# Kernel optimization log

Hardware: AMD Instinct MI355X
Metric: run time of the kernel (lower is better)

## Reference

```python
import jax, jax.numpy as jnp
import numpy as np

B, N, C = 2, 2048, 1024
H, D = 16, 64  # num_heads, dim_head; H*D == C
SCALE = D ** -0.5


def setup_inputs() -> dict:
    key = jax.random.key(0)
    ks = jax.random.split(key, 5)
    x = jax.random.normal(ks[0], (B, N, C), dtype=jnp.float32)
    attn_bias = jax.random.normal(ks[1], (B, H, N, N), dtype=jnp.float32)
    Wq = jax.random.normal(ks[2], (C, C), dtype=jnp.float32) * (C ** -0.5)
    Wkv = jax.random.normal(ks[3], (2 * C, C), dtype=jnp.float32) * (C ** -0.5)
    Wo = jax.random.normal(ks[4], (C, C), dtype=jnp.float32) * (C ** -0.5)
    bo = jnp.zeros((C,), dtype=jnp.float32)
    return {"x": x, "attn_bias": attn_bias, "Wq": Wq, "Wkv": Wkv, "Wo": Wo, "bo": bo}


def reference(x, attn_bias, Wq, Wkv, Wo, bo):
    # QKV projections (torch Linear: y = x @ W.T)
    q = (x @ Wq.T).reshape(B, N, H, D)
    kv = x @ Wkv.T  # self-attention: context = x
    k, v = jnp.split(kv, 2, axis=-1)
    k = k.reshape(B, N, H, D)
    v = v.reshape(B, N, H, D)
    # scores: [B, H, N, N]
    sim = jnp.einsum('bnhd,bmhd->bhnm', q, k) * SCALE + attn_bias
    attn = jax.nn.softmax(sim, axis=-1)
    out = jnp.einsum('bhnm,bmhd->bnhd', attn, v).reshape(B, N, C)
    return out @ Wo.T + bo
```

## Files before the change

### kernel.cpp

```cpp
#include <hip/hip_runtime.h>
#include <stdint.h>

#define BB 2
#define NN 2048
#define CC 1024
#define HH 16
#define DD 64

typedef unsigned short ushort_t;
using u16x8  = __attribute__((ext_vector_type(8))) unsigned short;
using bf16x8 = __attribute__((ext_vector_type(8))) __bf16;
using f32x4  = __attribute__((ext_vector_type(4))) float;

__device__ __forceinline__ unsigned short f2b(float f) {
  union { float f; uint32_t u; } v; v.f = f;
  uint32_t u = v.u;
  return (unsigned short)((u + 0x7fffu + ((u >> 16) & 1u)) >> 16);
}

__device__ __forceinline__ f32x4 mfma_bf16(u16x8 a, u16x8 b, f32x4 c) {
  return __builtin_amdgcn_mfma_f32_16x16x32_bf16(
      __builtin_bit_cast(bf16x8, a), __builtin_bit_cast(bf16x8, b), c, 0, 0, 0);
}

#define GLD_LDS16(gp, lp)                                                        \
  __builtin_amdgcn_global_load_lds(                                              \
      (const __attribute__((address_space(1))) void*)(gp),                       \
      (__attribute__((address_space(3))) void*)(lp), 16, 0, 0)

__global__ void cast_all(const float* __restrict__ x, const float* __restrict__ wq,
                         const float* __restrict__ wkv, const float* __restrict__ wo,
                         ushort_t* __restrict__ xb, ushort_t* __restrict__ wqb,
                         ushort_t* __restrict__ wkvb, ushort_t* __restrict__ wob) {
  int c = blockIdx.x * 256 + threadIdx.x;
  const float* src; ushort_t* dst; int off;
  if (c < 1048576)      { src = x;   dst = xb;   off = c; }
  else if (c < 1310720) { src = wq;  dst = wqb;  off = c - 1048576; }
  else if (c < 1835008) { src = wkv; dst = wkvb; off = c - 1310720; }
  else                  { src = wo;  dst = wob;  off = c - 1835008; }
  float4 v = *(const float4*)(src + (size_t)off * 4);
  ushort4 o;
  o.x = f2b(v.x); o.y = f2b(v.y); o.z = f2b(v.z); o.w = f2b(v.w);
  *(ushort4*)(dst + (size_t)off * 4) = o;
}

template <bool F32OUT>
__launch_bounds__(256, 2)
__global__ void gemm_bt(const ushort_t* __restrict__ A, const ushort_t* __restrict__ Bw,
                        void* __restrict__ out, const float* __restrict__ bo,
                        int M, int Nf, int K) {
  __shared__ __align__(16) ushort_t As[128 * 64];
  __shared__ __align__(16) ushort_t Bs[128 * 64];
  const int tid = threadIdx.x;
  const int w = tid >> 6, l = tid & 63;
  const int quad = l >> 4, l15 = l & 15;
  const int m0 = blockIdx.y * 128, n0 = blockIdx.x * 128;
  const int wm = (w >> 1) * 64, wn = (w & 1) * 64;

  const f32x4 zero = {0.f, 0.f, 0.f, 0.f};
  f32x4 acc[4][4];
  for (int i = 0; i < 4; ++i)
    for (int j = 0; j < 4; ++j) acc[i][j] = zero;

  for (int k0 = 0; k0 < K; k0 += 64) {
#pragma unroll
    for (int i = 0; i < 4; ++i) {
      int q = (i * 4 + w) * 64 + l;
      int row = q >> 3, c8 = (q & 7) * 8;
      GLD_LDS16(A + (size_t)(m0 + row) * K + k0 + c8, As + (i * 4 + w) * 512);
      GLD_LDS16(Bw + (size_t)(n0 + row) * K + k0 + c8, Bs + (i * 4 + w) * 512);
    }
    __syncthreads();
#pragma unroll
    for (int s = 0; s < 2; ++s) {
      u16x8 af[4], bf[4];
#pragma unroll
      for (int mi = 0; mi < 4; ++mi)
        af[mi] = *(const u16x8*)(As + (wm + mi * 16 + l15) * 64 + s * 32 + quad * 8);
#pragma unroll
      for (int ni = 0; ni < 4; ++ni)
        bf[ni] = *(const u16x8*)(Bs + (wn + ni * 16 + l15) * 64 + s * 32 + quad * 8);
#pragma unroll
      for (int mi = 0; mi < 4; ++mi)
#pragma unroll
        for (int ni = 0; ni < 4; ++ni)
          acc[mi][ni] = mfma_bf16(af[mi], bf[ni], acc[mi][ni]);
    }
    __syncthreads();
  }

#pragma unroll
  for (int mi = 0; mi < 4; ++mi) {
#pragma unroll
    for (int ni = 0; ni < 4; ++ni) {
      int col = n0 + wn + ni * 16 + l15;
      float badd = F32OUT ? bo[col] : 0.f;
#pragma unroll
      for (int r = 0; r < 4; ++r) {
        int row = m0 + wm + mi * 16 + quad * 4 + r;
        float v = acc[mi][ni][r] + badd;
        if (F32OUT) ((float*)out)[(size_t)row * Nf + col] = v;
        else        ((ushort_t*)out)[(size_t)row * Nf + col] = f2b(v);
      }
    }
  }
}

__launch_bounds__(256, 2)
__global__ void attn_fused(const ushort_t* __restrict__ qw,
                           const ushort_t* __restrict__ kvw,
                           const float* __restrict__ bias,
                           ushort_t* __restrict__ ao) {
  __shared__ __align__(16) ushort_t Qs[64 * 64];
  __shared__ __align__(16) ushort_t Ks[64 * 72];
  __shared__ __align__(16) ushort_t VTs[64 * 72];
  __shared__ __align__(16) ushort_t Ps[4 * 16 * 80];

  const int tid = threadIdx.x;
  const int w = tid >> 6, l = tid & 63;
  const int quad = l >> 4, l15 = l & 15;
  const int b = blockIdx.z, h = blockIdx.y;
  const int q0 = blockIdx.x * 64;

#pragma unroll
  for (int i = 0; i < 2; ++i) {
    int q = (w * 2 + i) * 64 + l;
    int row = q >> 3, c8 = (q & 7) * 8;
    GLD_LDS16(qw + ((size_t)(b * NN + q0 + row)) * CC + h * DD + c8,
              Qs + (w * 2 + i) * 512);
  }
  __syncthreads();

  u16x8 aq[2];
#pragma unroll
  for (int s = 0; s < 2; ++s)
    aq[s] = *(const u16x8*)(Qs + (w * 16 + l15) * 64 + s * 32 + quad * 8);

  const f32x4 zero = {0.f, 0.f, 0.f, 0.f};
  float m_run[4], l_run[4];
  f32x4 acc_o[4];
#pragma unroll
  for (int r = 0; r < 4; ++r) { m_run[r] = -1e30f; l_run[r] = 0.f; }
#pragma unroll
  for (int c = 0; c < 4; ++c) acc_o[c] = zero;

  const size_t bias_row0 = ((size_t)(b * HH + h)) * NN * NN;

  for (int kt = 0; kt < NN; kt += 64) {
#pragma unroll
    for (int i = 0; i < 2; ++i) {
      int chunk = i * 256 + tid;
      int key = chunk >> 3, c8 = (chunk & 7) * 8;
      const ushort_t* kp = kvw + ((size_t)(b * NN + kt + key)) * (2 * CC) + h * DD + c8;
      u16x8 k8 = *(const u16x8*)kp;
      *(u16x8*)(Ks + key * 72 + c8) = k8;
      u16x8 v8 = *(const u16x8*)(kp + CC);
#pragma unroll
      for (int j = 0; j < 8; ++j) VTs[(c8 + j) * 72 + key] = v8[j];
    }
    __syncthreads();

    float bv[4][4];
#pragma unroll
    for (int c = 0; c < 4; ++c)
#pragma unroll
      for (int r = 0; r < 4; ++r)
        bv[c][r] = bias[bias_row0 + (size_t)(q0 + w * 16 + quad * 4 + r) * NN +
                        kt + c * 16 + l15];

    f32x4 accs[4];
#pragma unroll
    for (int c = 0; c < 4; ++c) accs[c] = zero;
#pragma unroll
    for (int s = 0; s < 2; ++s)
#pragma unroll
      for (int c = 0; c < 4; ++c) {
        u16x8 bk = *(const u16x8*)(Ks + (c * 16 + l15) * 72 + s * 32 + quad * 8);
        accs[c] = mfma_bf16(aq[s], bk, accs[c]);
      }

#pragma unroll
    for (int r = 0; r < 4; ++r) {
      float sv[4];
      float mx = -1e30f;
#pragma unroll
      for (int c = 0; c < 4; ++c) {
        sv[c] = accs[c][r] * 0.125f + bv[c][r];
        mx = fmaxf(mx, sv[c]);
      }
#pragma unroll
      for (int off = 1; off < 16; off <<= 1)
        mx = fmaxf(mx, __shfl_xor(mx, off, 64));
      float mnew = fmaxf(m_run[r], mx);
      float alpha = __expf(m_run[r] - mnew);
      m_run[r] = mnew;
      float sum = 0.f;
#pragma unroll
      for (int c = 0; c < 4; ++c) {
        float pv = __expf(sv[c] - mnew);
        sum += pv;
        Ps[w * 1280 + (quad * 4 + r) * 80 + c * 16 + l15] = f2b(pv);
      }
#pragma unroll
      for (int off = 1; off < 16; off <<= 1)
        sum += __shfl_xor(sum, off, 64);
      l_run[r] = l_run[r] * alpha + sum;
#pragma unroll
      for (int c = 0; c < 4; ++c) acc_o[c][r] *= alpha;
    }

#pragma unroll
    for (int s = 0; s < 2; ++s) {
      u16x8 ap = *(const u16x8*)(Ps + w * 1280 + l15 * 80 + s * 32 + quad * 8);
#pragma unroll
      for (int c = 0; c < 4; ++c) {
        u16x8 vb = *(const u16x8*)(VTs + (c * 16 + l15) * 72 + s * 32 + quad * 8);
        acc_o[c] = mfma_bf16(ap, vb, acc_o[c]);
      }
    }
    __syncthreads();
  }

#pragma unroll
  for (int c = 0; c < 4; ++c)
#pragma unroll
    for (int r = 0; r < 4; ++r) {
      float v = acc_o[c][r] / l_run[r];
      int row = q0 + w * 16 + quad * 4 + r;
      ao[((size_t)(b * NN + row)) * CC + h * DD + c * 16 + l15] = f2b(v);
    }
}

extern "C" void kernel_launch(void* const* d_in, const int* in_sizes, int n_in,
                              void* d_out, int out_size, void* d_ws, size_t ws_size,
                              hipStream_t stream) {
  const float* x    = (const float*)d_in[0];
  const float* bias = (const float*)d_in[1];
  const float* Wq   = (const float*)d_in[2];
  const float* Wkv  = (const float*)d_in[3];
  const float* Wo   = (const float*)d_in[4];
  const float* bo   = (const float*)d_in[5];
  float* out = (float*)d_out;

  ushort_t* xb   = (ushort_t*)d_ws;
  ushort_t* wqb  = xb   + (size_t)4194304;
  ushort_t* wkvb = wqb  + (size_t)1048576;
  ushort_t* wob  = wkvb + (size_t)2097152;
  ushort_t* qws  = wob  + (size_t)1048576;
  ushort_t* kvws = qws  + (size_t)4194304;
  ushort_t* aow  = kvws + (size_t)8388608;

  cast_all<<<8192, 256, 0, stream>>>(x, Wq, Wkv, Wo, xb, wqb, wkvb, wob);
  gemm_bt<false><<<dim3(8, 32), 256, 0, stream>>>(xb, wqb, qws, nullptr, 4096, 1024, 1024);
  gemm_bt<false><<<dim3(16, 32), 256, 0, stream>>>(xb, wkvb, kvws, nullptr, 4096, 2048, 1024);
  attn_fused<<<dim3(32, 16, 2), 256, 0, stream>>>(qws, kvws, bias, aow);
  gemm_bt<true><<<dim3(8, 32), 256, 0, stream>>>(aow, wob, out, bo, 4096, 1024, 1024);
}
```

Before: 855.2 us.

## Write V transposed from KV GEMM and XOR-swizzle LDS tiles

The KV projection GEMM now writes K to its own buffer and writes V already transposed (per batch, dim by sequence). This lets the attention kernel load both K and V^T with async global-to-LDS copies instead of scalar transposing stores into LDS. All LDS tiles in the GEMM and attention kernels switch from padded rows to an XOR swizzle of 16-byte chunks to avoid bank conflicts, and the P buffer padding changes. The cost is strided 8-byte stores of V^T in the GEMM epilogue.

New measurement: 825.0 us. 3.5% less time.

```diff
diff --git a/kernel.cpp b/kernel.cpp
--- a/kernel.cpp
+++ b/kernel.cpp
@@ -27,6 +27,7 @@
   __builtin_amdgcn_global_load_lds(                                              \
       (const __attribute__((address_space(1))) void*)(gp),                       \
       (__attribute__((address_space(3))) void*)(lp), 16, 0, 0)
+
 
 __global__ void cast_all(const float* __restrict__ x, const float* __restrict__ wq,
                          const float* __restrict__ wkv, const float* __restrict__ wo,
@@ -44,11 +45,11 @@
   *(ushort4*)(dst + (size_t)off * 4) = o;
 }
 
-template <bool F32OUT>
+template <int MODE>
 __launch_bounds__(256, 2)
 __global__ void gemm_bt(const ushort_t* __restrict__ A, const ushort_t* __restrict__ Bw,
-                        void* __restrict__ out, const float* __restrict__ bo,
-                        int M, int Nf, int K) {
+                        void* __restrict__ out, ushort_t* __restrict__ vtw,
+                        const float* __restrict__ bo, int M, int Nf, int K) {
   __shared__ __align__(16) ushort_t As[128 * 64];
   __shared__ __align__(16) ushort_t Bs[128 * 64];
   const int tid = threadIdx.x;
@@ -66,27 +67,46 @@
 #pragma unroll
     for (int i = 0; i < 4; ++i) {
       int q = (i * 4 + w) * 64 + l;
-      int row = q >> 3, c8 = (q & 7) * 8;
-      GLD_LDS16(A + (size_t)(m0 + row) * K + k0 + c8, As + (i * 4 + w) * 512);
-      GLD_LDS16(Bw + (size_t)(n0 + row) * K + k0 + c8, Bs + (i * 4 + w) * 512);
+      int row = q >> 3;
+      int gc = (q & 7) ^ (row & 7);
+      GLD_LDS16(A + (size_t)(m0 + row) * K + k0 + gc * 8, As + (i * 4 + w) * 512);
+      GLD_LDS16(Bw + (size_t)(n0 + row) * K + k0 + gc * 8, Bs + (i * 4 + w) * 512);
     }
     __syncthreads();
 #pragma unroll
     for (int s = 0; s < 2; ++s) {
-      u16x8 af[4], bf[4];
+      u16x8 af[4], bf4[4];
+      const int slot = ((4 * s + quad) ^ (l15 & 7)) * 8;
 #pragma unroll
       for (int mi = 0; mi < 4; ++mi)
-        af[mi] = *(const u16x8*)(As + (wm + mi * 16 + l15) * 64 + s * 32 + quad * 8);
+        af[mi] = *(const u16x8*)(As + (wm + mi * 16 + l15) * 64 + slot);
 #pragma unroll
       for (int ni = 0; ni < 4; ++ni)
-        bf[ni] = *(const u16x8*)(Bs + (wn + ni * 16 + l15) * 64 + s * 32 + quad * 8);
+        bf4[ni] = *(const u16x8*)(Bs + (wn + ni * 16 + l15) * 64 + slot);
 #pragma unroll
       for (int mi = 0; mi < 4; ++mi)
 #pragma unroll
         for (int ni = 0; ni < 4; ++ni)
-          acc[mi][ni] = mfma_bf16(af[mi], bf[ni], acc[mi][ni]);
-    }
-    __syncthreads();
+          acc[mi][ni] = mfma_bf16(af[mi], bf4[ni], acc[mi][ni]);
+    }
+    __syncthreads();
+  }
+
+  if (MODE == 2 && n0 >= 1024) {
+#pragma unroll
+    for (int mi = 0; mi < 4; ++mi) {
+#pragma unroll
+      for (int ni = 0; ni < 4; ++ni) {
+        int d = n0 + wn + ni * 16 + l15 - 1024;
+        int row = m0 + wm + mi * 16 + quad * 4;
+        int b = row >> 11, n = row & 2047;
+        ushort4 p;
+        p.x = f2b(acc[mi][ni][0]); p.y = f2b(acc[mi][ni][1]);
+        p.z = f2b(acc[mi][ni][2]); p.w = f2b(acc[mi][ni][3]);
+        *(ushort4*)(vtw + ((size_t)(b * 1024 + d)) * 2048 + n) = p;
+      }
+    }
+    return;
   }
 
 #pragma unroll
@@ -94,13 +114,14 @@
 #pragma unroll
     for (int ni = 0; ni < 4; ++ni) {
       int col = n0 + wn + ni * 16 + l15;
-      float badd = F32OUT ? bo[col] : 0.f;
+      float badd = (MODE == 1) ? bo[col] : 0.f;
 #pragma unroll
       for (int r = 0; r < 4; ++r) {
         int row = m0 + wm + mi * 16 + quad * 4 + r;
         float v = acc[mi][ni][r] + badd;
-        if (F32OUT) ((float*)out)[(size_t)row * Nf + col] = v;
-        else        ((ushort_t*)out)[(size_t)row * Nf + col] = f2b(v);
+        if (MODE == 1)      ((float*)out)[(size_t)row * Nf + col] = v;
+        else if (MODE == 2) ((ushort_t*)out)[(size_t)row * 1024 + col] = f2b(v);
+        else                ((ushort_t*)out)[(size_t)row * Nf + col] = f2b(v);
       }
     }
   }
@@ -108,13 +129,14 @@
 
 __launch_bounds__(256, 2)
 __global__ void attn_fused(const ushort_t* __restrict__ qw,
-                           const ushort_t* __restrict__ kvw,
+                           const ushort_t* __restrict__ kw,
+                           const ushort_t* __restrict__ vtg,
                            const float* __restrict__ bias,
                            ushort_t* __restrict__ ao) {
   __shared__ __align__(16) ushort_t Qs[64 * 64];
-  __shared__ __align__(16) ushort_t Ks[64 * 72];
-  __shared__ __align__(16) ushort_t VTs[64 * 72];
-  __shared__ __align__(16) ushort_t Ps[4 * 16 * 80];
+  __shared__ __align__(16) ushort_t Ks[64 * 64];
+  __shared__ __align__(16) ushort_t VTs[64 * 64];
+  __shared__ __align__(16) ushort_t Ps[4 * 16 * 88];
 
   const int tid = threadIdx.x;
   const int w = tid >> 6, l = tid & 63;
@@ -122,11 +144,14 @@
   const int b = blockIdx.z, h = blockIdx.y;
   const int q0 = blockIdx.x * 64;
 
+  const ushort_t* vbase = vtg + ((size_t)(b * 1024 + h * 64)) * NN;
+
 #pragma unroll
   for (int i = 0; i < 2; ++i) {
     int q = (w * 2 + i) * 64 + l;
-    int row = q >> 3, c8 = (q & 7) * 8;
-    GLD_LDS16(qw + ((size_t)(b * NN + q0 + row)) * CC + h * DD + c8,
+    int row = q >> 3;
+    int gc = (q & 7) ^ (row & 7);
+    GLD_LDS16(qw + ((size_t)(b * NN + q0 + row)) * CC + h * DD + gc * 8,
               Qs + (w * 2 + i) * 512);
   }
   __syncthreads();
@@ -134,7 +159,7 @@
   u16x8 aq[2];
 #pragma unroll
   for (int s = 0; s < 2; ++s)
-    aq[s] = *(const u16x8*)(Qs + (w * 16 + l15) * 64 + s * 32 + quad * 8);
+    aq[s] = *(const u16x8*)(Qs + (w * 16 + l15) * 64 + (((4 * s + quad) ^ (l15 & 7)) * 8));
 
   const f32x4 zero = {0.f, 0.f, 0.f, 0.f};
   float m_run[4], l_run[4];
@@ -149,14 +174,13 @@
   for (int kt = 0; kt < NN; kt += 64) {
 #pragma unroll
     for (int i = 0; i < 2; ++i) {
-      int chunk = i * 256 + tid;
-      int key = chunk >> 3, c8 = (chunk & 7) * 8;
-      const ushort_t* kp = kvw + ((size_t)(b * NN + kt + key)) * (2 * CC) + h * DD + c8;
-      u16x8 k8 = *(const u16x8*)kp;
-      *(u16x8*)(Ks + key * 72 + c8) = k8;
-      u16x8 v8 = *(const u16x8*)(kp + CC);
-#pragma unroll
-      for (int j = 0; j < 8; ++j) VTs[(c8 + j) * 72 + key] = v8[j];
+      int q = i * 256 + tid;
+      int row = q >> 3;
+      int gc = (q & 7) ^ (row & 7);
+      GLD_LDS16(kw + ((size_t)(b * NN + kt + row)) * CC + h * DD + gc * 8,
+                Ks + i * 2048 + w * 512);
+      GLD_LDS16(vbase + (size_t)row * NN + kt + gc * 8,
+                VTs + i * 2048 + w * 512);
     }
     __syncthreads();
 
@@ -172,12 +196,14 @@
 #pragma unroll
     for (int c = 0; c < 4; ++c) accs[c] = zero;
 #pragma unroll
-    for (int s = 0; s < 2; ++s)
-#pragma unroll
-      for (int c = 0; c < 4; ++c) {
-        u16x8 bk = *(const u16x8*)(Ks + (c * 16 + l15) * 72 + s * 32 + quad * 8);
+    for (int s = 0; s < 2; ++s) {
+      const int slot = ((4 * s + quad) ^ (l15 & 7)) * 8;
+#pragma unroll
+      for (int c = 0; c < 4; ++c) {
+        u16x8 bk = *(const u16x8*)(Ks + (c * 16 + l15) * 64 + slot);
         accs[c] = mfma_bf16(aq[s], bk, accs[c]);
       }
+    }
 
 #pragma unroll
     for (int r = 0; r < 4; ++r) {
@@ -199,7 +225,7 @@
       for (int c = 0; c < 4; ++c) {
         float pv = __expf(sv[c] - mnew);
         sum += pv;
-        Ps[w * 1280 + (quad * 4 + r) * 80 + c * 16 + l15] = f2b(pv);
+        Ps[w * 1408 + (quad * 4 + r) * 88 + c * 16 + l15] = f2b(pv);
       }
 #pragma unroll
       for (int off = 1; off < 16; off <<= 1)
@@ -211,10 +237,11 @@
 
 #pragma unroll
     for (int s = 0; s < 2; ++s) {
-      u16x8 ap = *(const u16x8*)(Ps + w * 1280 + l15 * 80 + s * 32 + quad * 8);
-#pragma unroll
-      for (int c = 0; c < 4; ++c) {
-        u16x8 vb = *(const u16x8*)(VTs + (c * 16 + l15) * 72 + s * 32 + quad * 8);
+      u16x8 ap = *(const u16x8*)(Ps + w * 1408 + l15 * 88 + s * 32 + quad * 8);
+      const int slot = ((4 * s + quad) ^ (l15 & 7)) * 8;
+#pragma unroll
+      for (int c = 0; c < 4; ++c) {
+        u16x8 vb = *(const u16x8*)(VTs + (c * 16 + l15) * 64 + slot);
         acc_o[c] = mfma_bf16(ap, vb, acc_o[c]);
       }
     }
@@ -247,12 +274,13 @@
   ushort_t* wkvb = wqb  + (size_t)1048576;
   ushort_t* wob  = wkvb + (size_t)2097152;
   ushort_t* qws  = wob  + (size_t)1048576;
-  ushort_t* kvws = qws  + (size_t)4194304;
-  ushort_t* aow  = kvws + (size_t)8388608;
+  ushort_t* kws  = qws  + (size_t)4194304;
+  ushort_t* vtw  = kws  + (size_t)4194304;
+  ushort_t* aow  = vtw  + (size_t)4194304;
 
   cast_all<<<8192, 256, 0, stream>>>(x, Wq, Wkv, Wo, xb, wqb, wkvb, wob);
-  gemm_bt<false><<<dim3(8, 32), 256, 0, stream>>>(xb, wqb, qws, nullptr, 4096, 1024, 1024);
-  gemm_bt<false><<<dim3(16, 32), 256, 0, stream>>>(xb, wkvb, kvws, nullptr, 4096, 2048, 1024);
-  attn_fused<<<dim3(32, 16, 2), 256, 0, stream>>>(qws, kvws, bias, aow);
-  gemm_bt<true><<<dim3(8, 32), 256, 0, stream>>>(aow, wob, out, bo, 4096, 1024, 1024);
-}
+  gemm_bt<0><<<dim3(8, 32), 256, 0, stream>>>(xb, wqb, qws, nullptr, nullptr, 4096, 1024, 1024);
+  gemm_bt<2><<<dim3(16, 32), 256, 0, stream>>>(xb, wkvb, kws, vtw, nullptr, 4096, 2048, 1024);
+  attn_fused<<<dim3(32, 16, 2), 256, 0, stream>>>(qws, kws, vtw, bias, aow);
+  gemm_bt<1><<<dim3(8, 32), 256, 0, stream>>>(aow, wob, out, nullptr, bo, 4096, 1024, 1024);
+}
```
